# Kernel tuning notes

Hardware: AMD Instinct MI355X
Metric: run time of the kernel (lower is better)

## Reference

```python
import jax, jax.numpy as jnp
import numpy as np

CASCADES = 3
D, H, W = 64, 256, 256
HID = 8  # BasicBlock hidden channels


def fdiff(x, axis):
    """Forward difference D x along `axis` (last entry 0) == sparse dx/dy/dz matmul."""
    axis = axis % x.ndim
    pad = [(0, 0)] * x.ndim
    pad[axis] = (0, 1)
    return jnp.pad(jnp.diff(x, axis=axis), pad)


def fdiff_t(y, axis):
    """Exact transpose D^T y of fdiff: (D^T y)_0=-y_0, (D^T y)_j=y_{j-1}-y_j, (D^T y)_{n-1}=y_{n-2}."""
    axis = axis % y.ndim
    n = y.shape[axis]
    yl = jax.lax.slice_in_dim(y, 0, n - 1, axis=axis)  # y[0..n-2]
    pf = [(0, 0)] * y.ndim; pf[axis] = (1, 0)
    pb = [(0, 0)] * y.ndim; pb[axis] = (0, 1)
    return jnp.pad(yl, pf) - jnp.pad(yl, pb)


def conv3d(x, w, b):
    out = jax.lax.conv_general_dilated(
        x, w, window_strides=(1, 1, 1), padding='SAME',
        dimension_numbers=('NCDHW', 'OIDHW', 'NCDHW'))
    return out + b[None, :, None, None, None]


def basic_block(x, w1, b1, w2, b2):
    h = jax.nn.relu(conv3d(x, w1, b1))
    return conv3d(h, w2, b2), jnp.mean(jnp.abs(h))


def ite(t, sino):
    """BeijingGeometry stand-in: one SIRT-style step A^T(sino - A t)/D, A = sum over depth."""
    proj = jnp.sum(t, axis=2)               # [B,1,H,W]
    res = sino - proj
    return jnp.broadcast_to(res[:, :, None], t.shape) / t.shape[2]


def setup_inputs() -> dict:
    key = jax.random.key(0)
    ks = jax.random.split(key, 8)
    image = jax.random.normal(ks[0], (1, 1, D, H, W), dtype=jnp.float32)
    sino = jax.random.normal(ks[1], (1, 1, H, W), dtype=jnp.float32)
    # 4 BasicBlocks stacked on leading axis
    W1 = jax.random.normal(ks[2], (4, HID, 1, 3, 3, 3), dtype=jnp.float32) * 0.1
    B1 = jnp.zeros((4, HID), dtype=jnp.float32)
    W2 = jax.random.normal(ks[3], (4, 1, HID, 3, 3, 3), dtype=jnp.float32) * 0.1
    B2 = jnp.zeros((4, 1), dtype=jnp.float32)
    ntx = jnp.full((CASCADES,), -0.01, dtype=jnp.float32)
    nty = jnp.full((CASCADES,), -0.01, dtype=jnp.float32)
    ntz = jnp.full((CASCADES,), -0.01, dtype=jnp.float32)
    nt = jnp.full((CASCADES,), -0.1, dtype=jnp.float32)
    return {"image": image, "sino": sino, "W1": W1, "B1": B1, "W2": W2, "B2": B2,
            "ntx": ntx, "nty": nty, "ntz": ntz, "nt": nt}


def reference(image, sino, W1, B1, W2, B2, ntx, nty, ntz, nt):
    t = image
    p = q = s = jnp.float32(0.0)
    outs = [image]
    for c in range(CASCADES):
        z = t + ite(t, sino)
        pnew, _ = basic_block(fdiff(z, -1), W1[0], B1[0], W2[0], B2[0])  # d/dx (W axis)
        qnew, _ = basic_block(fdiff(z, -2), W1[1], B1[1], W2[1], B2[1])  # d/dy (H axis)
        snew, _ = basic_block(fdiff(z, -3), W1[2], B1[2], W2[2], B2[2])  # d/dz (D axis)
        znew, _ = basic_block(z, W1[3], B1[3], W2[3], B2[3])
        p = p + ntx[c] * (p - pnew)
        q = q + nty[c] * (q - qnew)
        s = s + ntz[c] * (s - snew)
        z_ = t + nt[c] * (t - znew)
        t = fdiff_t(p, -1) + fdiff_t(q, -2) + fdiff_t(s, -3) + z_
        outs.append(t)
    return jnp.stack(outs, axis=0)  # [cascades+1, B, 1, D, H, W]
```

## Files before the change

### kernel.cpp

```cpp
#include <hip/hip_runtime.h>

#define DD 64
#define HH 256
#define WW 256
#define HW (HH * WW)
#define NVOX (DD * HW)

#define TS 32
#define DR 36
#define HR 34
#define HP 34
#define CHB 22
#define NPF 6

__global__ __launch_bounds__(256) void k_corr(const float* __restrict__ t,
                                              const float* __restrict__ sino,
                                              float* __restrict__ corr) {
  int idx = blockIdx.x * 256 + threadIdx.x;
  float s = 0.f;
#pragma unroll 8
  for (int d = 0; d < DD; ++d) s += t[d * HW + idx];
  corr[idx] = (sino[idx] - s) * (1.0f / DD);
}

__global__ __launch_bounds__(256, 3) void k_blocks(
    const float* __restrict__ t, const float* __restrict__ corr,
    float* __restrict__ p, float* __restrict__ q, float* __restrict__ s_,
    float* __restrict__ zb,
    const float* __restrict__ W1g, const float* __restrict__ B1g,
    const float* __restrict__ W2g, const float* __restrict__ B2g,
    const float* __restrict__ ntx, const float* __restrict__ nty,
    const float* __restrict__ ntz, const float* __restrict__ nt, int c) {
  __shared__ __align__(16) float dbuf[3][DR][DR];
  __shared__ __align__(16) float hbuf[8][HR][HP];

  const int b = blockIdx.z & 3;
  const int D0 = (blockIdx.z >> 2) * CHB;
  const int Dend = (D0 + CHB < DD) ? (D0 + CHB) : DD;
  const int ty0 = blockIdx.y * TS;
  const int tx0 = blockIdx.x * TS;
  const int tid = threadIdx.x;

  const float* w1 = W1g + b * 216;
  const float* w2 = W2g + b * 216;
  float b1[8];
#pragma unroll
  for (int ch = 0; ch < 8; ++ch) b1[ch] = B1g[b * 8 + ch];
  const float b2 = B2g[b];
  const float coef = (b == 0) ? ntx[c] : (b == 1) ? nty[c] : (b == 2) ? ntz[c] : nt[c];
  const float* prevBuf = (b == 0) ? p : (b == 1) ? q : (b == 2) ? s_ : t;
  float* outBuf = (b == 0) ? p : (b == 1) ? q : (b == 2) ? s_ : zb;
  const bool zeroPrev = (c == 0) && (b < 3);

  auto dslot = [](int f) { return (f + 6) % 3; };

  float pA0[NPF], pA1[NPF], pC0[NPF], pC1[NPF];

  auto issue_loads = [&](int f) {
#pragma unroll
    for (int k = 0; k < NPF; ++k) {
      int i = tid + k * 256;
      pA0[k] = 0.f; pA1[k] = 0.f; pC0[k] = 0.f; pC1[k] = 0.f;
      if (i < DR * DR) {
        int iy = i / DR, ix = i - iy * DR;
        int gy = ty0 - 2 + iy, gx = tx0 - 2 + ix;
        if (f >= 0 && f < DD && (unsigned)gy < HH && (unsigned)gx < WW) {
          int base = f * HW + gy * WW + gx;
          int cb = gy * WW + gx;
          if (b == 0) {
            if (gx + 1 < WW) { pA0[k] = t[base]; pA1[k] = t[base + 1];
                               pC0[k] = corr[cb]; pC1[k] = corr[cb + 1]; }
          } else if (b == 1) {
            if (gy + 1 < HH) { pA0[k] = t[base]; pA1[k] = t[base + WW];
                               pC0[k] = corr[cb]; pC1[k] = corr[cb + WW]; }
          } else if (b == 2) {
            if (f + 1 < DD) { pA0[k] = t[base]; pA1[k] = t[base + HW]; }
          } else {
            pA0[k] = t[base]; pC0[k] = corr[cb];
          }
        }
      }
    }
  };
  auto write_deriv = [&](int f) {
    float* dst = &dbuf[dslot(f)][0][0];
#pragma unroll
    for (int k = 0; k < NPF; ++k) {
      int i = tid + k * 256;
      if (i < DR * DR) {
        float v;
        if (b == 3) v = pA0[k] + pC0[k];
        else v = (pA1[k] - pA0[k]) + (pC1[k] - pC0[k]);
        dst[i] = v;
      }
    }
  };

  auto conv1_patch = [&](const float* d0, const float* d1, const float* d2,
                         int jy, int jx, int ch0, int ch1) {
    float win[3][4][4];
#pragma unroll
    for (int r = 0; r < 4; ++r) {
      int off = (jy + r) * DR + jx;
      const float2* r0 = (const float2*)(d0 + off);
      const float2* r1 = (const float2*)(d1 + off);
      const float2* r2 = (const float2*)(d2 + off);
      float2 a, bb;
      a = r0[0]; bb = r0[1];
      win[0][r][0] = a.x; win[0][r][1] = a.y; win[0][r][2] = bb.x; win[0][r][3] = bb.y;
      a = r1[0]; bb = r1[1];
      win[1][r][0] = a.x; win[1][r][1] = a.y; win[1][r][2] = bb.x; win[1][r][3] = bb.y;
      a = r2[0]; bb = r2[1];
      win[2][r][0] = a.x; win[2][r][1] = a.y; win[2][r][2] = bb.x; win[2][r][3] = bb.y;
    }
    int gy0 = ty0 - 1 + jy, gx0 = tx0 - 1 + jx;
    bool in00 = ((unsigned)gy0 < HH) && ((unsigned)gx0 < WW);
    bool in01 = ((unsigned)gy0 < HH) && ((unsigned)(gx0 + 1) < WW);
    bool in10 = ((unsigned)(gy0 + 1) < HH) && ((unsigned)gx0 < WW);
    bool in11 = ((unsigned)(gy0 + 1) < HH) && ((unsigned)(gx0 + 1) < WW);
#pragma unroll 2
    for (int ch = ch0; ch < ch1; ++ch) {
      float bia = b1[ch];
      float a00 = bia, a01 = bia, a10 = bia, a11 = bia;
      const float* wch = w1 + ch * 27;
#pragma unroll
      for (int kz = 0; kz < 3; ++kz)
#pragma unroll
        for (int ky = 0; ky < 3; ++ky)
#pragma unroll
          for (int kx = 0; kx < 3; ++kx) {
            float wv = wch[kz * 9 + ky * 3 + kx];
            a00 = fmaf(wv, win[kz][ky][kx], a00);
            a01 = fmaf(wv, win[kz][ky][kx + 1], a01);
            a10 = fmaf(wv, win[kz][ky + 1][kx], a10);
            a11 = fmaf(wv, win[kz][ky + 1][kx + 1], a11);
          }
      float2 r0v, r1v;
      r0v.x = in00 ? fmaxf(a00, 0.f) : 0.f;
      r0v.y = in01 ? fmaxf(a01, 0.f) : 0.f;
      r1v.x = in10 ? fmaxf(a10, 0.f) : 0.f;
      r1v.y = in11 ? fmaxf(a11, 0.f) : 0.f;
      *(float2*)&hbuf[ch][jy][jx] = r0v;
      *(float2*)&hbuf[ch][jy + 1][jx] = r1v;
    }
  };

  auto comp_hidden = [&](int e) {
    const float* d0 = &dbuf[dslot(e - 1)][0][0];
    const float* d1 = &dbuf[dslot(e)][0][0];
    const float* d2 = &dbuf[dslot(e + 1)][0][0];
    {
      int prr = tid / 17, pcc = tid - prr * 17;
      conv1_patch(d0, d1, d2, prr * 2, pcc * 2, 0, 8);
    }
    if (tid < 132) {
      int m = tid >> 2, chp = (tid & 3) << 1;
      int pi = 256 + m;
      int prr = pi / 17, pcc = pi - prr * 17;
      conv1_patch(d0, d1, d2, prr * 2, pcc * 2, chp, chp + 2);
    }
  };

  const int txi = tid & 15, tyi = tid >> 4;
  const int px0 = txi * 2, py0 = tyi * 2;

  float aM[2][2], aC[2][2], aP[2][2];
#pragma unroll
  for (int i = 0; i < 2; ++i)
#pragma unroll
    for (int j = 0; j < 2; ++j) { aM[i][j] = b2; aC[i][j] = b2; aP[i][j] = b2; }

  issue_loads(D0 - 2); write_deriv(D0 - 2);
  issue_loads(D0 - 1); write_deriv(D0 - 1);
  issue_loads(D0);     write_deriv(D0);
  __syncthreads();

  for (int e = D0 - 1; e <= Dend; ++e) {
    const bool live = (e >= 0 && e < DD);
    issue_loads(e + 2);
    float2 pr0, pr1;
    pr0.x = pr0.y = pr1.x = pr1.y = 0.f;
    const int d = e - 1;
    const bool doStore = (e >= D0 + 1);
    if (doStore && !zeroPrev) {
      size_t v0 = (size_t)d * HW + (size_t)(ty0 + py0) * WW + tx0 + px0;
      pr0 = *(const float2*)&prevBuf[v0];
      pr1 = *(const float2*)&prevBuf[v0 + WW];
    }
    if (live) comp_hidden(e);
    __syncthreads();
    if (live) {
#pragma unroll 1
      for (int ch = 0; ch < 8; ++ch) {
        float hwf[4][4];
#pragma unroll
        for (int r = 0; r < 4; ++r) {
          const float2* row = (const float2*)&hbuf[ch][py0 + r][px0];
          float2 a0 = row[0], a1 = row[1];
          hwf[r][0] = a0.x; hwf[r][1] = a0.y; hwf[r][2] = a1.x; hwf[r][3] = a1.y;
        }
        const float* wch = w2 + ch * 27;
#pragma unroll
        for (int ky = 0; ky < 3; ++ky)
#pragma unroll
          for (int kx = 0; kx < 3; ++kx) {
            float w0 = wch[0 + ky * 3 + kx];
            float w1v = wch[9 + ky * 3 + kx];
            float w2v = wch[18 + ky * 3 + kx];
#pragma unroll
            for (int i = 0; i < 2; ++i)
#pragma unroll
              for (int j = 0; j < 2; ++j) {
                float h = hwf[i + ky][j + kx];
                aP[i][j] = fmaf(w0, h, aP[i][j]);
                aC[i][j] = fmaf(w1v, h, aC[i][j]);
                aM[i][j] = fmaf(w2v, h, aM[i][j]);
              }
          }
      }
    }
    write_deriv(e + 2);
    if (doStore) {
      size_t v0 = (size_t)d * HW + (size_t)(ty0 + py0) * WW + tx0 + px0;
      float2 o0, o1;
      o0.x = pr0.x + coef * (pr0.x - aM[0][0]);
      o0.y = pr0.y + coef * (pr0.y - aM[0][1]);
      o1.x = pr1.x + coef * (pr1.x - aM[1][0]);
      o1.y = pr1.y + coef * (pr1.y - aM[1][1]);
      *(float2*)&outBuf[v0] = o0;
      *(float2*)&outBuf[v0 + WW] = o1;
    }
#pragma unroll
    for (int i = 0; i < 2; ++i)
#pragma unroll
      for (int j = 0; j < 2; ++j) {
        aM[i][j] = aC[i][j]; aC[i][j] = aP[i][j]; aP[i][j] = b2;
      }
    __syncthreads();
  }
}

__global__ __launch_bounds__(256) void k_combine(
    const float* __restrict__ p, const float* __restrict__ q,
    const float* __restrict__ s_, const float* __restrict__ zb,
    float* __restrict__ tn) {
  int idx = blockIdx.x * 256 + threadIdx.x;
  int x = idx & (WW - 1);
  int y = (idx >> 8) & (HH - 1);
  int d = idx >> 16;
  float v = zb[idx];
  v += (x > 0 ? p[idx - 1] : 0.f) - (x < WW - 1 ? p[idx] : 0.f);
  v += (y > 0 ? q[idx - WW] : 0.f) - (y < HH - 1 ? q[idx] : 0.f);
  v += (d > 0 ? s_[idx - HW] : 0.f) - (d < DD - 1 ? s_[idx] : 0.f);
  tn[idx] = v;
}

extern "C" void kernel_launch(void* const* d_in, const int* in_sizes, int n_in,
                              void* d_out, int out_size, void* d_ws, size_t ws_size,
                              hipStream_t stream) {
  const float* image = (const float*)d_in[0];
  const float* sino  = (const float*)d_in[1];
  const float* W1    = (const float*)d_in[2];
  const float* B1    = (const float*)d_in[3];
  const float* W2    = (const float*)d_in[4];
  const float* B2    = (const float*)d_in[5];
  const float* ntx   = (const float*)d_in[6];
  const float* nty   = (const float*)d_in[7];
  const float* ntz   = (const float*)d_in[8];
  const float* nt    = (const float*)d_in[9];
  float* out = (float*)d_out;

  float* corr = (float*)d_ws;
  float* p  = corr + HW;
  float* q  = p + NVOX;
  float* s_ = q + NVOX;
  float* zb = s_ + NVOX;

  hipMemcpyAsync(out, image, (size_t)NVOX * sizeof(float),
                 hipMemcpyDeviceToDevice, stream);

  for (int c = 0; c < 3; ++c) {
    const float* t = out + (size_t)c * NVOX;
    float* tn = out + (size_t)(c + 1) * NVOX;
    k_corr<<<HW / 256, 256, 0, stream>>>(t, sino, corr);
    k_blocks<<<dim3(WW / TS, HH / TS, 12), 256, 0, stream>>>(
        t, corr, p, q, s_, zb, W1, B1, W2, B2, ntx, nty, ntz, nt, c);
    k_combine<<<NVOX / 256, 256, 0, stream>>>(p, q, s_, zb, tn);
  }
}
```

Before: 958.2 us.

## Store hidden activations in fp16 LDS, precompute corr deltas, raise occupancy

Hidden-layer activations in shared memory are now stored as fp16 instead of fp32, roughly halving that buffer so four blocks can fit per CU (launch bounds 4, depth chunk 16, grid z 16). The per-voxel corr loads and index math are hoisted out of the depth loop into precomputed offsets, deltas and a validity bitmask, which cuts global loads and integer work per slice. The intent is to raise occupancy and reduce load pressure. The cost is reduced precision in the intermediate activations and more halo recomputation from the smaller depth chunks.

```diff
diff --git a/kernel.cpp b/kernel.cpp
--- a/kernel.cpp
+++ b/kernel.cpp
@@ -8,10 +8,11 @@
 
 #define TS 32
 #define DR 36
-#define HR 34
-#define HP 34
-#define CHB 22
+#define HPH 40
+#define CHB 16
 #define NPF 6
+
+typedef __fp16 half2v __attribute__((ext_vector_type(2)));
 
 __global__ __launch_bounds__(256) void k_corr(const float* __restrict__ t,
                                               const float* __restrict__ sino,
@@ -23,7 +24,7 @@
   corr[idx] = (sino[idx] - s) * (1.0f / DD);
 }
 
-__global__ __launch_bounds__(256, 3) void k_blocks(
+__global__ __launch_bounds__(256, 4) void k_blocks(
     const float* __restrict__ t, const float* __restrict__ corr,
     float* __restrict__ p, float* __restrict__ q, float* __restrict__ s_,
     float* __restrict__ zb,
@@ -32,7 +33,7 @@
     const float* __restrict__ ntx, const float* __restrict__ nty,
     const float* __restrict__ ntz, const float* __restrict__ nt, int c) {
   __shared__ __align__(16) float dbuf[3][DR][DR];
-  __shared__ __align__(16) float hbuf[8][HR][HP];
+  __shared__ __align__(16) __fp16 hbuf[8][34][HPH];
 
   const int b = blockIdx.z & 3;
   const int D0 = (blockIdx.z >> 2) * CHB;
@@ -51,34 +52,51 @@
   const float* prevBuf = (b == 0) ? p : (b == 1) ? q : (b == 2) ? s_ : t;
   float* outBuf = (b == 0) ? p : (b == 1) ? q : (b == 2) ? s_ : zb;
   const bool zeroPrev = (c == 0) && (b < 3);
+  const int strideA = (b == 0) ? 1 : (b == 1) ? WW : HW;
 
   auto dslot = [](int f) { return (f + 6) % 3; };
 
-  float pA0[NPF], pA1[NPF], pC0[NPF], pC1[NPF];
+  int cbt[NPF];
+  float dC[NPF];
+  unsigned mbits = 0;
+#pragma unroll
+  for (int k = 0; k < NPF; ++k) {
+    int i = tid + k * 256;
+    int iy = i / DR, ix = i - iy * DR;
+    int gy = ty0 - 2 + iy, gx = tx0 - 2 + ix;
+    bool inb = (i < DR * DR) && ((unsigned)gy < HH) && ((unsigned)gx < WW);
+    int cb = gy * WW + gx;
+    cbt[k] = cb;
+    bool m;
+    float d = 0.f;
+    if (b == 0) {
+      m = inb && (gx + 1 < WW);
+      if (m) d = corr[cb + 1] - corr[cb];
+    } else if (b == 1) {
+      m = inb && (gy + 1 < HH);
+      if (m) d = corr[cb + WW] - corr[cb];
+    } else if (b == 2) {
+      m = inb;
+    } else {
+      m = inb;
+      if (m) d = corr[cb];
+    }
+    dC[k] = d;
+    if (m) mbits |= (1u << k);
+  }
+
+  float pA0[NPF], pA1[NPF];
 
   auto issue_loads = [&](int f) {
+    const bool fok = (f >= 0) && (f < DD) && (b != 2 || (f + 1 < DD));
+    const int fb = f * HW;
 #pragma unroll
     for (int k = 0; k < NPF; ++k) {
-      int i = tid + k * 256;
-      pA0[k] = 0.f; pA1[k] = 0.f; pC0[k] = 0.f; pC1[k] = 0.f;
-      if (i < DR * DR) {
-        int iy = i / DR, ix = i - iy * DR;
-        int gy = ty0 - 2 + iy, gx = tx0 - 2 + ix;
-        if (f >= 0 && f < DD && (unsigned)gy < HH && (unsigned)gx < WW) {
-          int base = f * HW + gy * WW + gx;
-          int cb = gy * WW + gx;
-          if (b == 0) {
-            if (gx + 1 < WW) { pA0[k] = t[base]; pA1[k] = t[base + 1];
-                               pC0[k] = corr[cb]; pC1[k] = corr[cb + 1]; }
-          } else if (b == 1) {
-            if (gy + 1 < HH) { pA0[k] = t[base]; pA1[k] = t[base + WW];
-                               pC0[k] = corr[cb]; pC1[k] = corr[cb + WW]; }
-          } else if (b == 2) {
-            if (f + 1 < DD) { pA0[k] = t[base]; pA1[k] = t[base + HW]; }
-          } else {
-            pA0[k] = t[base]; pC0[k] = corr[cb];
-          }
-        }
+      pA0[k] = 0.f; pA1[k] = 0.f;
+      if (fok && ((mbits >> k) & 1u)) {
+        const float* base = t + fb + cbt[k];
+        pA0[k] = base[0];
+        if (b != 3) pA1[k] = base[strideA];
       }
     }
   };
@@ -86,12 +104,9 @@
     float* dst = &dbuf[dslot(f)][0][0];
 #pragma unroll
     for (int k = 0; k < NPF; ++k) {
-      int i = tid + k * 256;
-      if (i < DR * DR) {
-        float v;
-        if (b == 3) v = pA0[k] + pC0[k];
-        else v = (pA1[k] - pA0[k]) + (pC1[k] - pC0[k]);
-        dst[i] = v;
+      if (k < 5 || tid < (DR * DR - 5 * 256)) {
+        float v = (b == 3) ? (pA0[k] + dC[k]) : ((pA1[k] - pA0[k]) + dC[k]);
+        dst[tid + k * 256] = v;
       }
     }
   };
@@ -135,13 +150,13 @@
             a10 = fmaf(wv, win[kz][ky + 1][kx], a10);
             a11 = fmaf(wv, win[kz][ky + 1][kx + 1], a11);
           }
-      float2 r0v, r1v;
-      r0v.x = in00 ? fmaxf(a00, 0.f) : 0.f;
-      r0v.y = in01 ? fmaxf(a01, 0.f) : 0.f;
-      r1v.x = in10 ? fmaxf(a10, 0.f) : 0.f;
-      r1v.y = in11 ? fmaxf(a11, 0.f) : 0.f;
-      *(float2*)&hbuf[ch][jy][jx] = r0v;
-      *(float2*)&hbuf[ch][jy + 1][jx] = r1v;
+      half2v h0, h1;
+      h0.x = (__fp16)(in00 ? fmaxf(a00, 0.f) : 0.f);
+      h0.y = (__fp16)(in01 ? fmaxf(a01, 0.f) : 0.f);
+      h1.x = (__fp16)(in10 ? fmaxf(a10, 0.f) : 0.f);
+      h1.y = (__fp16)(in11 ? fmaxf(a11, 0.f) : 0.f);
+      *(half2v*)&hbuf[ch][jy][jx] = h0;
+      *(half2v*)&hbuf[ch][jy + 1][jx] = h1;
     }
   };
 
@@ -195,9 +210,11 @@
         float hwf[4][4];
 #pragma unroll
         for (int r = 0; r < 4; ++r) {
-          const float2* row = (const float2*)&hbuf[ch][py0 + r][px0];
-          float2 a0 = row[0], a1 = row[1];
-          hwf[r][0] = a0.x; hwf[r][1] = a0.y; hwf[r][2] = a1.x; hwf[r][3] = a1.y;
+          const __fp16* hp = &hbuf[ch][py0 + r][px0];
+          half2v a0 = *(const half2v*)hp;
+          half2v a1 = *(const half2v*)(hp + 2);
+          hwf[r][0] = (float)a0.x; hwf[r][1] = (float)a0.y;
+          hwf[r][2] = (float)a1.x; hwf[r][3] = (float)a1.y;
         }
         const float* wch = w2 + ch * 27;
 #pragma unroll
@@ -283,7 +300,7 @@
     const float* t = out + (size_t)c * NVOX;
     float* tn = out + (size_t)(c + 1) * NVOX;
     k_corr<<<HW / 256, 256, 0, stream>>>(t, sino, corr);
-    k_blocks<<<dim3(WW / TS, HH / TS, 12), 256, 0, stream>>>(
+    k_blocks<<<dim3(WW / TS, HH / TS, 16), 256, 0, stream>>>(
         t, corr, p, q, s_, zb, W1, B1, W2, B2, ntx, nty, ntz, nt, c);
     k_combine<<<NVOX / 256, 256, 0, stream>>>(p, q, s_, zb, tn);
   }
```

Measured after the change: 942.0 us (median of 2 runs). About the same (-1.7%).
